# Kernel tuning notes

Measured on AMD Instinct MI355X. Metric: run time of the kernel, lower is better.

## Reference

```python
import jax, jax.numpy as jnp
import numpy as np

N_NODES = 100000
N_EDGES = 1600000
D_IN = 128
D_MSG = 128
D_HID = 128
D_EDGE = 5
D_CAT = D_IN + D_MSG  # 256
D_U1, D_U2, D_OUT = 214, 172, 128  # delta = (256-128)//3 = 42


def _leaky(x):
    return jax.nn.leaky_relu(x, negative_slope=0.01)


def setup_inputs() -> dict:
    key = jax.random.key(0)
    ks = jax.random.split(key, 12)
    def kaiming(k, shape):
        fan_in = shape[1]
        gain = np.sqrt(2.0 / (1.0 + 0.01 ** 2))
        return jax.random.normal(k, shape, dtype=jnp.float32) * (gain / np.sqrt(fan_in))
    x = jax.random.normal(ks[0], (N_NODES, D_IN), dtype=jnp.float32)
    edge_index = jax.random.randint(ks[1], (2, N_EDGES), 0, N_NODES, dtype=jnp.int64)
    edge_attr = jax.random.normal(ks[2], (N_EDGES, D_EDGE), dtype=jnp.float32)
    return {
        "x": x, "edge_index": edge_index, "edge_attr": edge_attr,
        "Wm1": kaiming(ks[3], (D_HID, D_EDGE)), "bm1": jnp.zeros((D_HID,), jnp.float32),
        "Wm2": kaiming(ks[4], (D_HID, D_HID)), "bm2": jnp.zeros((D_HID,), jnp.float32),
        "Wm3": kaiming(ks[5], (D_MSG, D_HID)), "bm3": jnp.zeros((D_MSG,), jnp.float32),
        "ln_g": jnp.ones((D_CAT,), jnp.float32), "ln_b": jnp.zeros((D_CAT,), jnp.float32),
        "Wu1": kaiming(ks[6], (D_U1, D_CAT)), "bu1": jnp.zeros((D_U1,), jnp.float32),
        "Wu2": kaiming(ks[7], (D_U2, D_U1)), "bu2": jnp.zeros((D_U2,), jnp.float32),
        "Wu3": kaiming(ks[8], (D_OUT, D_U2)), "bu3": jnp.zeros((D_OUT,), jnp.float32),
    }


def reference(x, edge_index, edge_attr, Wm1, bm1, Wm2, bm2, Wm3, bm3,
              ln_g, ln_b, Wu1, bu1, Wu2, bu2, Wu3, bu3):
    # --- message: MLP2 on edge_attr only ---  [E, D_MSG]
    h = _leaky(edge_attr @ Wm1.T + bm1)
    h = _leaky(h @ Wm2.T + bm2)
    msg = h @ Wm3.T + bm3
    # --- aggregate: scatter-add per destination node (edge_index[1]) ---
    dst = edge_index[1]
    aggr = jax.ops.segment_sum(msg, dst, num_segments=x.shape[0])  # [N, D_MSG]
    # --- update: LayerNorm(concat) then shrinking MLP ---
    cat = jnp.concatenate([x, aggr], axis=-1)  # [N, 256]
    mu = jnp.mean(cat, axis=-1, keepdims=True)
    var = jnp.mean((cat - mu) ** 2, axis=-1, keepdims=True)
    nrm = (cat - mu) * jax.lax.rsqrt(var + 1e-5) * ln_g + ln_b
    u = _leaky(nrm @ Wu1.T + bu1)
    u = _leaky(u @ Wu2.T + bu2)
    return u @ Wu3.T + bu3  # [N, D_OUT]
```

## Files before the change

### kernel.cpp

```cpp
#include <hip/hip_runtime.h>

#define N_NODES 100000
#define N_EDGES 1600000
#define STRN 264
#define NBLK_SCAN 391

typedef __attribute__((ext_vector_type(4))) float floatx4;
typedef __attribute__((ext_vector_type(8))) __bf16 bf16x8;
typedef __attribute__((ext_vector_type(8))) unsigned short ushort8;
typedef __attribute__((ext_vector_type(4))) unsigned short ushort4v;

#define WS_AGGR   0ull
#define WS_COUNTS 51200000ull
#define WS_OFFS   51600384ull
#define WS_PART   52000768ull
#define WS_DSTS   52002816ull
#define WS_ATTRS  58402816ull
#define WS_W2     90402816ull
#define WS_W3     (WS_W2 + 32768ull)
#define WS_WU1    (WS_W3 + 32768ull)
#define WS_WU2    (WS_WU1 + 114688ull)
#define WS_WU3    (WS_WU2 + 86016ull)

__device__ __forceinline__ unsigned short tobf(float f) {
  return __builtin_bit_cast(unsigned short, (__bf16)f);
}

__device__ __forceinline__ float leaky(float v) { return fmaxf(v, 0.01f * v); }

__device__ __forceinline__ int swz(int row, int ch) {
  return row * 128 + (ch ^ ((row & 7) << 3));
}

__device__ __forceinline__ int msw(int e, int ch) {
  return e * 16 + (ch ^ (((e >> 1) & 3) << 2));
}

__global__ void prep_kernel(const float* __restrict__ Wm2, const float* __restrict__ Wm3,
                            const float* __restrict__ Wu1, const float* __restrict__ Wu2,
                            const float* __restrict__ Wu3,
                            unsigned short* __restrict__ o2, unsigned short* __restrict__ o3,
                            unsigned short* __restrict__ o1p, unsigned short* __restrict__ o2p,
                            unsigned short* __restrict__ o3p) {
  int i = blockIdx.x * 256 + threadIdx.x;
  if (i < 16384) {
    o2[i] = tobf(Wm2[i]);
  } else if (i < 32768) {
    int j = i - 16384; o3[j] = tobf(Wm3[j]);
  } else if (i < 32768 + 57344) {
    int j = i - 32768; int n = j >> 8, k = j & 255;
    o1p[j] = (n < 214) ? tobf(Wu1[n * 256 + k]) : (unsigned short)0;
  } else if (i < 90112 + 43008) {
    int j = i - 90112; int n = j / 224, k = j - n * 224;
    o2p[j] = (n < 172 && k < 214) ? tobf(Wu2[n * 214 + k]) : (unsigned short)0;
  } else if (i < 133120 + 24576) {
    int j = i - 133120; int n = j / 192, k = j - n * 192;
    o3p[j] = (k < 172) ? tobf(Wu3[n * 172 + k]) : (unsigned short)0;
  }
}

__global__ void hist_kernel(const int* __restrict__ dst, int* __restrict__ counts) {
  int e = blockIdx.x * 256 + threadIdx.x;
  if (e < N_EDGES) atomicAdd(&counts[dst[e]], 1);
}

__global__ void scanA_kernel(const int* __restrict__ counts, int* __restrict__ offs,
                             int* __restrict__ partials) {
  __shared__ int tmp[256];
  const int t = threadIdx.x;
  const int i = blockIdx.x * 256 + t;
  int v = (i < N_NODES) ? counts[i] : 0;
  tmp[t] = v;
  __syncthreads();
  for (int off = 1; off < 256; off <<= 1) {
    int a = (t >= off) ? tmp[t - off] : 0;
    __syncthreads();
    tmp[t] += a;
    __syncthreads();
  }
  if (i < N_NODES) offs[i] = tmp[t] - v;
  if (t == 255) partials[blockIdx.x] = tmp[255];
}

__global__ void scanB_kernel(int* __restrict__ partials) {
  __shared__ int tmp[512];
  const int t = threadIdx.x;
  int v = (t < NBLK_SCAN) ? partials[t] : 0;
  tmp[t] = v;
  __syncthreads();
  for (int off = 1; off < 512; off <<= 1) {
    int a = (t >= off) ? tmp[t - off] : 0;
    __syncthreads();
    tmp[t] += a;
    __syncthreads();
  }
  if (t < NBLK_SCAN) partials[t] = tmp[t] - v;
}

__global__ void scanC_kernel(int* __restrict__ offs, const int* __restrict__ partials) {
  int i = blockIdx.x * 256 + threadIdx.x;
  if (i < N_NODES) offs[i] += partials[blockIdx.x];
}

__global__ void scatter_kernel(const int* __restrict__ dst, int* __restrict__ offs,
                               const float* __restrict__ attr,
                               float* __restrict__ attrS, int* __restrict__ dsts) {
  int e = blockIdx.x * 256 + threadIdx.x;
  if (e < N_EDGES) {
    int d = dst[e];
    int p = atomicAdd(&offs[d], 1);
    dsts[p] = d;
    const float* a = attr + (size_t)e * 5;
    float a0 = a[0], a1 = a[1], a2 = a[2], a3 = a[3], a4 = a[4];
    float* o = attrS + (size_t)p * 5;
    o[0] = a0; o[1] = a1; o[2] = a2; o[3] = a3; o[4] = a4;
  }
}

__global__ __launch_bounds__(256, 4) void edge_kernel(
    const float* __restrict__ attrS, const int* __restrict__ dsts,
    const float* __restrict__ Wm1, const float* __restrict__ bm1,
    const unsigned short* __restrict__ W2bf, const float* __restrict__ bm2,
    const unsigned short* __restrict__ W3bf, const float* __restrict__ bm3,
    float* __restrict__ aggr) {
  __shared__ __align__(16) char smem[39424];
  unsigned short* sH = (unsigned short*)(void*)smem;
  float* sMsg = (float*)(void*)smem;
  float* sAttr8 = (float*)(void*)(smem + 32768);
  float* sWm1F = (float*)(void*)(smem + 36864);

  const int t = threadIdx.x;
  const int wave = t >> 6, lane = t & 63;
  const int col = lane & 15, q = lane >> 4;
  const int eb = wave * 32;
  const int wbase = wave * 32;
  const long blockEdge = (long)blockIdx.x * 128;

  for (int i = t; i < 640; i += 256) {
    sWm1F[i] = Wm1[i];
    float v = attrS[blockEdge * 5 + i];
    int e = i / 5, j = i - e * 5;
    sAttr8[e * 8 + j] = v;
  }
  const int dE0 = dsts[blockEdge + q * 32 + col];
  const int dE1 = dsts[blockEdge + q * 32 + 16 + col];
  __syncthreads();

  {
    const int c = lane;
    const float* wa = sWm1F + c * 5;
    const float* wb = sWm1F + (c + 64) * 5;
    float wa0 = wa[0], wa1 = wa[1], wa2 = wa[2], wa3 = wa[3], wa4 = wa[4];
    float wb0 = wb[0], wb1 = wb[1], wb2 = wb[2], wb3 = wb[3], wb4 = wb[4];
    float ba = bm1[c], bb = bm1[c + 64];
#pragma unroll 4
    for (int e = 0; e < 32; e++) {
      const float* ar = sAttr8 + (eb + e) * 8;
      float4 a = *(const float4*)ar;
      float a4 = ar[4];
      float ha = fmaf(a.x, wa0, fmaf(a.y, wa1, fmaf(a.z, wa2, fmaf(a.w, wa3, fmaf(a4, wa4, ba)))));
      float hb = fmaf(a.x, wb0, fmaf(a.y, wb1, fmaf(a.z, wb2, fmaf(a.w, wb3, fmaf(a4, wb4, bb)))));
      sH[swz(eb + e, c)] = tobf(leaky(ha));
      sH[swz(eb + e, c + 64)] = tobf(leaky(hb));
    }
  }
  __syncthreads();

  floatx4 acc[2][8];

  {
    bf16x8 w2f[2][4];
#pragma unroll
    for (int i = 0; i < 2; i++)
#pragma unroll
      for (int ks = 0; ks < 4; ks++)
        w2f[i][ks] = *(const bf16x8*)(const void*)
            &W2bf[(wbase + i * 16 + col) * 128 + ks * 32 + q * 8];
#pragma unroll
    for (int i = 0; i < 2; i++)
#pragma unroll
      for (int j = 0; j < 8; j++) acc[i][j] = (floatx4){0.f, 0.f, 0.f, 0.f};
#pragma unroll
    for (int ks = 0; ks < 4; ks++) {
      const int kk = ks * 32 + q * 8;
#pragma unroll
      for (int et = 0; et < 8; et++) {
        bf16x8 hb = *(const bf16x8*)(const void*)&sH[swz(et * 16 + col, kk)];
        acc[0][et] = __builtin_amdgcn_mfma_f32_16x16x32_bf16(w2f[0][ks], hb, acc[0][et], 0, 0, 0);
        acc[1][et] = __builtin_amdgcn_mfma_f32_16x16x32_bf16(w2f[1][ks], hb, acc[1][et], 0, 0, 0);
      }
    }
  }
  __syncthreads();

  {
    float4 b2lo = *(const float4*)&bm2[wbase + q * 4];
    float4 b2hi = *(const float4*)&bm2[wbase + 16 + q * 4];
#pragma unroll
    for (int et = 0; et < 8; et++) {
      const int e = et * 16 + col;
#pragma unroll
      for (int r = 0; r < 4; r++) {
        sH[swz(e, wbase + q * 4 + r)] = tobf(leaky(acc[0][et][r] + ((const float*)&b2lo)[r]));
        sH[swz(e, wbase + 16 + q * 4 + r)] = tobf(leaky(acc[1][et][r] + ((const float*)&b2hi)[r]));
      }
    }
  }
  __syncthreads();

  {
    bf16x8 w3f[2][4];
#pragma unroll
    for (int i = 0; i < 2; i++)
#pragma unroll
      for (int ks = 0; ks < 4; ks++)
        w3f[i][ks] = *(const bf16x8*)(const void*)
            &W3bf[(wbase + i * 16 + col) * 128 + ks * 32 + q * 8];
#pragma unroll
    for (int i = 0; i < 2; i++)
#pragma unroll
      for (int j = 0; j < 8; j++) acc[i][j] = (floatx4){0.f, 0.f, 0.f, 0.f};
#pragma unroll
    for (int ks = 0; ks < 4; ks++) {
      const int kk = ks * 32 + q * 8;
#pragma unroll
      for (int et = 0; et < 8; et++) {
        bf16x8 hb = *(const bf16x8*)(const void*)&sH[swz(et * 16 + col, kk)];
        acc[0][et] = __builtin_amdgcn_mfma_f32_16x16x32_bf16(w3f[0][ks], hb, acc[0][et], 0, 0, 0);
        acc[1][et] = __builtin_amdgcn_mfma_f32_16x16x32_bf16(w3f[1][ks], hb, acc[1][et], 0, 0, 0);
      }
    }
  }
  __syncthreads();

  const int wslab = wave * 2048;
#pragma unroll
  for (int c = 0; c < 2; c++) {
    float4 b3 = *(const float4*)&bm3[wbase + c * 16 + q * 4];
#pragma unroll
    for (int et = 0; et < 8; et++) {
      const int e = et * 16 + col;
#pragma unroll
      for (int r = 0; r < 4; r++)
        sMsg[wslab + msw(e, q * 4 + r)] = acc[c][et][r] + ((const float*)&b3)[r];
    }
    asm volatile("s_waitcnt lgkmcnt(0)" ::: "memory");

    const int ch = col;
    const int chG = wbase + c * 16 + ch;
    float accv = 0.f;
    int dprev = __shfl(dE0, lane & 48);
#pragma unroll 8
    for (int it = 0; it < 32; it++) {
      int d = __shfl((it < 16) ? dE0 : dE1, (lane & 48) + (it & 15));
      float v = sMsg[wslab + msw(q * 32 + it, ch)];
      if (d != dprev) {
        atomicAdd(&aggr[(size_t)dprev * 128 + chG], accv);
        accv = 0.f;
        dprev = d;
      }
      accv += v;
    }
    atomicAdd(&aggr[(size_t)dprev * 128 + chG], accv);
  }
}

template <int TILES, int CT, int KST, bool FINAL>
__device__ __forceinline__ void layer_node_sw(unsigned short* __restrict__ sX,
                                              const unsigned short* __restrict__ W,
                                              const float* __restrict__ bias, int biasLim,
                                              int wave, int lane, int nodeGBase,
                                              float* __restrict__ out) {
  const int col = lane & 15, q = lane >> 4;
  const int K = KST * 32;
  floatx4 acc[CT][4];
#pragma unroll
  for (int c = 0; c < CT; c++)
#pragma unroll
    for (int n = 0; n < 4; n++) acc[c][n] = (floatx4){0.f, 0.f, 0.f, 0.f};

#pragma unroll
  for (int ks = 0; ks < KST; ks++) {
    const int kk = ks * 32 + q * 8;
    bf16x8 a[CT];
#pragma unroll
    for (int c = 0; c < CT; c++) {
      const int tile = wave + 4 * c;
      const int tc = (tile < TILES) ? tile : 0;
      a[c] = *(const bf16x8*)(const void*)&W[(tc * 16 + col) * K + kk];
    }
    bf16x8 b[4];
#pragma unroll
    for (int n = 0; n < 4; n++)
      b[n] = *(const bf16x8*)(const void*)&sX[(n * 16 + col) * STRN + kk];
#pragma unroll
    for (int c = 0; c < CT; c++) {
      if (wave + 4 * c < TILES) {
#pragma unroll
        for (int n = 0; n < 4; n++)
          acc[c][n] = __builtin_amdgcn_mfma_f32_16x16x32_bf16(a[c], b[n], acc[c][n], 0, 0, 0);
      }
    }
  }
  __syncthreads();

#pragma unroll
  for (int c = 0; c < CT; c++) {
    const int tile = wave + 4 * c;
    if (tile < TILES) {
      float bv[4];
#pragma unroll
      for (int r = 0; r < 4; r++) {
        const int ch = tile * 16 + q * 4 + r;
        bv[r] = (ch < biasLim) ? bias[ch] : 0.f;
      }
#pragma unroll
      for (int n = 0; n < 4; n++) {
        const int node = n * 16 + col;
        if (!FINAL) {
          ushort4v p;
#pragma unroll
          for (int r = 0; r < 4; r++) p[r] = tobf(leaky(acc[c][n][r] + bv[r]));
          *(ushort4v*)(void*)&sX[node * STRN + tile * 16 + q * 4] = p;
        } else {
          const long ng = (long)nodeGBase + node;
          if (ng < N_NODES) {
            float4 p = make_float4(acc[c][n][0] + bv[0], acc[c][n][1] + bv[1],
                                   acc[c][n][2] + bv[2], acc[c][n][3] + bv[3]);
            *(float4*)(void*)&out[ng * 128 + tile * 16 + q * 4] = p;
          }
        }
      }
    }
  }
  if (!FINAL) __syncthreads();
}

__global__ __launch_bounds__(256, 4) void node_kernel(
    const float* __restrict__ x, const float* __restrict__ aggr,
    const float* __restrict__ lng, const float* __restrict__ lnb,
    const unsigned short* __restrict__ Wu1p, const float* __restrict__ bu1,
    const unsigned short* __restrict__ Wu2p, const float* __restrict__ bu2,
    const unsigned short* __restrict__ Wu3p, const float* __restrict__ bu3,
    float* __restrict__ out) {
  __shared__ unsigned short sX[64 * STRN];
  __shared__ float sG[256], sB[256];
  const int t = threadIdx.x;
  const int wave = t >> 6, lane = t & 63;
  sG[t] = lng[t];
  sB[t] = lnb[t];

  const int nl = t >> 2;
  const int part = t & 3;
  const long nodeG = (long)blockIdx.x * 64 + nl;
  const bool valid = nodeG < N_NODES;
  const float* src = (part < 2) ? (x + nodeG * 128 + part * 64)
                                : (aggr + nodeG * 128 + (part - 2) * 64);
  float s = 0.f, ss = 0.f;
  if (valid) {
#pragma unroll
    for (int i = 0; i < 16; i++) {
      float4 a = *(const float4*)(src + i * 4);
      s += a.x + a.y + a.z + a.w;
      ss += a.x * a.x + a.y * a.y + a.z * a.z + a.w * a.w;
    }
  }
  s += __shfl_xor(s, 1); s += __shfl_xor(s, 2);
  ss += __shfl_xor(ss, 1); ss += __shfl_xor(ss, 2);
  const float mean = s * (1.f / 256.f);
  const float var = ss * (1.f / 256.f) - mean * mean;
  const float rstd = rsqrtf(var + 1e-5f);
  __syncthreads();
  const int cb = part * 64;
#pragma unroll
  for (int i = 0; i < 16; i++) {
    float4 a = valid ? *(const float4*)(src + i * 4) : make_float4(0.f, 0.f, 0.f, 0.f);
    int c = cb + i * 4;
    ushort4v p;
    p[0] = tobf((a.x - mean) * rstd * sG[c + 0] + sB[c + 0]);
    p[1] = tobf((a.y - mean) * rstd * sG[c + 1] + sB[c + 1]);
    p[2] = tobf((a.z - mean) * rstd * sG[c + 2] + sB[c + 2]);
    p[3] = tobf((a.w - mean) * rstd * sG[c + 3] + sB[c + 3]);
    *(ushort4v*)(void*)&sX[nl * STRN + c] = p;
  }
  __syncthreads();

  const int nodeGBase = blockIdx.x * 64;
  layer_node_sw<14, 4, 8, false>(sX, Wu1p, bu1, 214, wave, lane, nodeGBase, nullptr);
  layer_node_sw<12, 3, 7, false>(sX, Wu2p, bu2, 172, wave, lane, nodeGBase, nullptr);
  layer_node_sw<8, 2, 6, true>(sX, Wu3p, bu3, 128, wave, lane, nodeGBase, out);
}

extern "C" void kernel_launch(void* const* d_in, const int* in_sizes, int n_in,
                              void* d_out, int out_size, void* d_ws, size_t ws_size,
                              hipStream_t stream) {
  const float* x    = (const float*)d_in[0];
  const int*   eidx = (const int*)d_in[1];
  const float* attr = (const float*)d_in[2];
  const float* Wm1  = (const float*)d_in[3];
  const float* bm1  = (const float*)d_in[4];
  const float* Wm2  = (const float*)d_in[5];
  const float* bm2  = (const float*)d_in[6];
  const float* Wm3  = (const float*)d_in[7];
  const float* bm3  = (const float*)d_in[8];
  const float* lng  = (const float*)d_in[9];
  const float* lnb  = (const float*)d_in[10];
  const float* Wu1  = (const float*)d_in[11];
  const float* bu1  = (const float*)d_in[12];
  const float* Wu2  = (const float*)d_in[13];
  const float* bu2  = (const float*)d_in[14];
  const float* Wu3  = (const float*)d_in[15];
  const float* bu3  = (const float*)d_in[16];
  float* out = (float*)d_out;

  char* ws = (char*)d_ws;
  float* aggr  = (float*)(ws + WS_AGGR);
  int* counts  = (int*)(ws + WS_COUNTS);
  int* offs    = (int*)(ws + WS_OFFS);
  int* parts   = (int*)(ws + WS_PART);
  int* dsts    = (int*)(ws + WS_DSTS);
  float* attrS = (float*)(ws + WS_ATTRS);
  unsigned short* W2bf = (unsigned short*)(ws + WS_W2);
  unsigned short* W3bf = (unsigned short*)(ws + WS_W3);
  unsigned short* Wu1p = (unsigned short*)(ws + WS_WU1);
  unsigned short* Wu2p = (unsigned short*)(ws + WS_WU2);
  unsigned short* Wu3p = (unsigned short*)(ws + WS_WU3);

  const int* dst = eidx + N_EDGES;

  hipMemsetAsync(counts, 0, 400384, stream);
  hist_kernel<<<6250, 256, 0, stream>>>(dst, counts);
  scanA_kernel<<<NBLK_SCAN, 256, 0, stream>>>(counts, offs, parts);
  scanB_kernel<<<1, 512, 0, stream>>>(parts);
  scanC_kernel<<<NBLK_SCAN, 256, 0, stream>>>(offs, parts);
  scatter_kernel<<<6250, 256, 0, stream>>>(dst, offs, attr, attrS, dsts);

  hipMemsetAsync(aggr, 0, (size_t)N_NODES * 128 * sizeof(float), stream);
  prep_kernel<<<616, 256, 0, stream>>>(Wm2, Wm3, Wu1, Wu2, Wu3, W2bf, W3bf, Wu1p, Wu2p, Wu3p);

  edge_kernel<<<N_EDGES / 128, 256, 0, stream>>>(attrS, dsts, Wm1, bm1, W2bf, bm2, W3bf,
                                                 bm3, aggr);
  node_kernel<<<(N_NODES + 63) / 64, 256, 0, stream>>>(x, aggr, lng, lnb, Wu1p, bu1, Wu2p, bu2,
                                                       Wu3p, bu3, out);
}
```

Baseline: 697.3 us.

## Accumulate edge messages with fixed-point integer atomics; halve node-kernel tile

Messages are scaled by 4096 and rounded to int before the segmented atomic adds, so aggregation runs on integer atomics instead of float atomics. The node kernel converts the ints back to float when it reads them. The node kernel also drops from 64 to 32 nodes per block, using 2 MFMA column tiles instead of 4 and half the LDS, which doubles the grid. The change trades precision (quantization to 1/4096, possible int overflow for large sums) for cheaper atomics, and gives up some weight reuse per block in exchange for more blocks.

```diff
diff --git a/kernel.cpp b/kernel.cpp
--- a/kernel.cpp
+++ b/kernel.cpp
@@ -4,6 +4,9 @@
 #define N_EDGES 1600000
 #define STRN 264
 #define NBLK_SCAN 391
+
+#define MSG_SCALE 4096.0f
+#define MSG_INV   0.000244140625f
 
 typedef __attribute__((ext_vector_type(4))) float floatx4;
 typedef __attribute__((ext_vector_type(8))) __bf16 bf16x8;
@@ -122,7 +125,7 @@
     const float* __restrict__ Wm1, const float* __restrict__ bm1,
     const unsigned short* __restrict__ W2bf, const float* __restrict__ bm2,
     const unsigned short* __restrict__ W3bf, const float* __restrict__ bm3,
-    float* __restrict__ aggr) {
+    int* __restrict__ aggr) {
   __shared__ __align__(16) char smem[39424];
   unsigned short* sH = (unsigned short*)(void*)smem;
   float* sMsg = (float*)(void*)smem;
@@ -248,18 +251,19 @@
 
     const int ch = col;
     const int chG = wbase + c * 16 + ch;
-    float accv = 0.f;
+    int accv = 0;
     int dprev = __shfl(dE0, lane & 48);
 #pragma unroll 8
     for (int it = 0; it < 32; it++) {
       int d = __shfl((it < 16) ? dE0 : dE1, (lane & 48) + (it & 15));
       float v = sMsg[wslab + msw(q * 32 + it, ch)];
+      int iv = __float2int_rn(v * MSG_SCALE);
       if (d != dprev) {
         atomicAdd(&aggr[(size_t)dprev * 128 + chG], accv);
-        accv = 0.f;
+        accv = 0;
         dprev = d;
       }
-      accv += v;
+      accv += iv;
     }
     atomicAdd(&aggr[(size_t)dprev * 128 + chG], accv);
   }
@@ -273,11 +277,11 @@
                                               float* __restrict__ out) {
   const int col = lane & 15, q = lane >> 4;
   const int K = KST * 32;
-  floatx4 acc[CT][4];
+  floatx4 acc[CT][2];
 #pragma unroll
   for (int c = 0; c < CT; c++)
 #pragma unroll
-    for (int n = 0; n < 4; n++) acc[c][n] = (floatx4){0.f, 0.f, 0.f, 0.f};
+    for (int n = 0; n < 2; n++) acc[c][n] = (floatx4){0.f, 0.f, 0.f, 0.f};
 
 #pragma unroll
   for (int ks = 0; ks < KST; ks++) {
@@ -289,15 +293,15 @@
       const int tc = (tile < TILES) ? tile : 0;
       a[c] = *(const bf16x8*)(const void*)&W[(tc * 16 + col) * K + kk];
     }
-    bf16x8 b[4];
-#pragma unroll
-    for (int n = 0; n < 4; n++)
+    bf16x8 b[2];
+#pragma unroll
+    for (int n = 0; n < 2; n++)
       b[n] = *(const bf16x8*)(const void*)&sX[(n * 16 + col) * STRN + kk];
 #pragma unroll
     for (int c = 0; c < CT; c++) {
       if (wave + 4 * c < TILES) {
 #pragma unroll
-        for (int n = 0; n < 4; n++)
+        for (int n = 0; n < 2; n++)
           acc[c][n] = __builtin_amdgcn_mfma_f32_16x16x32_bf16(a[c], b[n], acc[c][n], 0, 0, 0);
       }
     }
@@ -315,7 +319,7 @@
         bv[r] = (ch < biasLim) ? bias[ch] : 0.f;
       }
 #pragma unroll
-      for (int n = 0; n < 4; n++) {
+      for (int n = 0; n < 2; n++) {
         const int node = n * 16 + col;
         if (!FINAL) {
           ushort4v p;
@@ -337,13 +341,13 @@
 }
 
 __global__ __launch_bounds__(256, 4) void node_kernel(
-    const float* __restrict__ x, const float* __restrict__ aggr,
+    const float* __restrict__ x, const int* __restrict__ aggr,
     const float* __restrict__ lng, const float* __restrict__ lnb,
     const unsigned short* __restrict__ Wu1p, const float* __restrict__ bu1,
     const unsigned short* __restrict__ Wu2p, const float* __restrict__ bu2,
     const unsigned short* __restrict__ Wu3p, const float* __restrict__ bu3,
     float* __restrict__ out) {
-  __shared__ unsigned short sX[64 * STRN];
+  __shared__ unsigned short sX[32 * STRN];
   __shared__ float sG[256], sB[256];
   const int t = threadIdx.x;
   const int wave = t >> 6, lane = t & 63;
@@ -352,15 +356,21 @@
 
   const int nl = t >> 2;
   const int part = t & 3;
-  const long nodeG = (long)blockIdx.x * 64 + nl;
-  const bool valid = nodeG < N_NODES;
-  const float* src = (part < 2) ? (x + nodeG * 128 + part * 64)
-                                : (aggr + nodeG * 128 + (part - 2) * 64);
+  const long nodeG = (long)blockIdx.x * 32 + nl;
+  const bool valid = (t < 128) && (nodeG < N_NODES);
+  const float* srcF = x + nodeG * 128 + part * 64;
+  const int* srcI = aggr + nodeG * 128 + (part - 2) * 64;
   float s = 0.f, ss = 0.f;
   if (valid) {
 #pragma unroll
     for (int i = 0; i < 16; i++) {
-      float4 a = *(const float4*)(src + i * 4);
+      float4 a;
+      if (part < 2) {
+        a = *(const float4*)(srcF + i * 4);
+      } else {
+        int4 iv = *(const int4*)(srcI + i * 4);
+        a = make_float4(iv.x * MSG_INV, iv.y * MSG_INV, iv.z * MSG_INV, iv.w * MSG_INV);
+      }
       s += a.x + a.y + a.z + a.w;
       ss += a.x * a.x + a.y * a.y + a.z * a.z + a.w * a.w;
     }
@@ -371,21 +381,29 @@
   const float var = ss * (1.f / 256.f) - mean * mean;
   const float rstd = rsqrtf(var + 1e-5f);
   __syncthreads();
-  const int cb = part * 64;
-#pragma unroll
-  for (int i = 0; i < 16; i++) {
-    float4 a = valid ? *(const float4*)(src + i * 4) : make_float4(0.f, 0.f, 0.f, 0.f);
-    int c = cb + i * 4;
-    ushort4v p;
-    p[0] = tobf((a.x - mean) * rstd * sG[c + 0] + sB[c + 0]);
-    p[1] = tobf((a.y - mean) * rstd * sG[c + 1] + sB[c + 1]);
-    p[2] = tobf((a.z - mean) * rstd * sG[c + 2] + sB[c + 2]);
-    p[3] = tobf((a.w - mean) * rstd * sG[c + 3] + sB[c + 3]);
-    *(ushort4v*)(void*)&sX[nl * STRN + c] = p;
-  }
-  __syncthreads();
-
-  const int nodeGBase = blockIdx.x * 64;
+  if (valid) {
+    const int cb = part * 64;
+#pragma unroll
+    for (int i = 0; i < 16; i++) {
+      float4 a;
+      if (part < 2) {
+        a = *(const float4*)(srcF + i * 4);
+      } else {
+        int4 iv = *(const int4*)(srcI + i * 4);
+        a = make_float4(iv.x * MSG_INV, iv.y * MSG_INV, iv.z * MSG_INV, iv.w * MSG_INV);
+      }
+      int c = cb + i * 4;
+      ushort4v p;
+      p[0] = tobf((a.x - mean) * rstd * sG[c + 0] + sB[c + 0]);
+      p[1] = tobf((a.y - mean) * rstd * sG[c + 1] + sB[c + 1]);
+      p[2] = tobf((a.z - mean) * rstd * sG[c + 2] + sB[c + 2]);
+      p[3] = tobf((a.w - mean) * rstd * sG[c + 3] + sB[c + 3]);
+      *(ushort4v*)(void*)&sX[nl * STRN + c] = p;
+    }
+  }
+  __syncthreads();
+
+  const int nodeGBase = blockIdx.x * 32;
   layer_node_sw<14, 4, 8, false>(sX, Wu1p, bu1, 214, wave, lane, nodeGBase, nullptr);
   layer_node_sw<12, 3, 7, false>(sX, Wu2p, bu2, 172, wave, lane, nodeGBase, nullptr);
   layer_node_sw<8, 2, 6, true>(sX, Wu3p, bu3, 128, wave, lane, nodeGBase, out);
@@ -414,7 +432,7 @@
   float* out = (float*)d_out;
 
   char* ws = (char*)d_ws;
-  float* aggr  = (float*)(ws + WS_AGGR);
+  int* aggr    = (int*)(ws + WS_AGGR);
   int* counts  = (int*)(ws + WS_COUNTS);
   int* offs    = (int*)(ws + WS_OFFS);
   int* parts   = (int*)(ws + WS_PART);
@@ -435,11 +453,11 @@
   scanC_kernel<<<NBLK_SCAN, 256, 0, stream>>>(offs, parts);
   scatter_kernel<<<6250, 256, 0, stream>>>(dst, offs, attr, attrS, dsts);
 
-  hipMemsetAsync(aggr, 0, (size_t)N_NODES * 128 * sizeof(float), stream);
+  hipMemsetAsync(aggr, 0, (size_t)N_NODES * 128 * sizeof(int), stream);
   prep_kernel<<<616, 256, 0, stream>>>(Wm2, Wm3, Wu1, Wu2, Wu3, W2bf, W3bf, Wu1p, Wu2p, Wu3p);
 
   edge_kernel<<<N_EDGES / 128, 256, 0, stream>>>(attrS, dsts, Wm1, bm1, W2bf, bm2, W3bf,
                                                  bm3, aggr);
-  node_kernel<<<(N_NODES + 63) / 64, 256, 0, stream>>>(x, aggr, lng, lnb, Wu1p, bu1, Wu2p, bu2,
+  node_kernel<<<(N_NODES + 31) / 32, 256, 0, stream>>>(x, aggr, lng, lnb, Wu1p, bu1, Wu2p, bu2,
                                                        Wu3p, bu3, out);
 }
```

Result: slower. 731.2 us (+4.9%).
